# Kernel tuning notes

Hardware: AMD Instinct MI355X
Metric: run time of the kernel (lower is better)

The kernel has to match this reference:

```python
import jax, jax.numpy as jnp
import numpy as np

N = 100000
NEG_SLOPE = 0.2
EPS = 1e-16


def gat_conv(x, edge_index, W, att_src, att_dst, bias, concat):
    # x: [N, Fin]; W: [Fin, H*C]; att_*: [H, C]; edge_index: [2, E] (with self loops)
    H, C = att_src.shape
    src, dst = edge_index[0], edge_index[1]
    h = (x @ W).reshape(-1, H, C)                       # [N, H, C]
    a_src = (h * att_src).sum(-1)                       # [N, H]
    a_dst = (h * att_dst).sum(-1)                       # [N, H]
    e = a_src[src] + a_dst[dst]                         # [E, H]
    e = jnp.where(e >= 0, e, NEG_SLOPE * e)             # LeakyReLU(0.2)
    # segment softmax over destination-node neighborhoods
    m = jax.ops.segment_max(e, dst, num_segments=N)     # [N, H]
    ex = jnp.exp(e - m[dst])
    denom = jax.ops.segment_sum(ex, dst, num_segments=N)
    alpha = ex / (denom[dst] + EPS)                     # [E, H]
    msg = h[src] * alpha[:, :, None]                    # [E, H, C]
    out = jax.ops.segment_sum(msg, dst, num_segments=N)  # [N, H, C]
    out = out.reshape(N, H * C) if concat else out.mean(axis=1)
    return out + bias


def setup_inputs() -> dict:
    key = jax.random.key(0)
    ks = jax.random.split(key, 10)
    Fin, Ch, Co, Hh = 256, 32, 64, 4
    E = 1600000
    x = jax.random.normal(ks[0], (N, Fin), dtype=jnp.float32)
    edge_index = jax.random.randint(ks[1], (2, E), 0, N, dtype=jnp.int64)
    s1 = 1.0 / np.sqrt(Fin)
    s2 = 1.0 / np.sqrt(Hh * Ch)
    W1 = jax.random.normal(ks[2], (Fin, Hh * Ch), dtype=jnp.float32) * s1
    att_src1 = jax.random.normal(ks[3], (Hh, Ch), dtype=jnp.float32) * (1.0 / np.sqrt(Ch))
    att_dst1 = jax.random.normal(ks[4], (Hh, Ch), dtype=jnp.float32) * (1.0 / np.sqrt(Ch))
    b1 = jnp.zeros((Hh * Ch,), dtype=jnp.float32)
    W2 = jax.random.normal(ks[5], (Hh * Ch, Co), dtype=jnp.float32) * s2
    att_src2 = jax.random.normal(ks[6], (1, Co), dtype=jnp.float32) * (1.0 / np.sqrt(Co))
    att_dst2 = jax.random.normal(ks[7], (1, Co), dtype=jnp.float32) * (1.0 / np.sqrt(Co))
    b2 = jnp.zeros((Co,), dtype=jnp.float32)
    return {"x": x, "edge_index": edge_index,
            "W1": W1, "att_src1": att_src1, "att_dst1": att_dst1, "b1": b1,
            "W2": W2, "att_src2": att_src2, "att_dst2": att_dst2, "b2": b2}


def reference(x, edge_index, W1, att_src1, att_dst1, b1, W2, att_src2, att_dst2, b2):
    # add self-loops (PyG GATConv default add_self_loops=True)
    loops = jnp.arange(N, dtype=edge_index.dtype)
    ei = jnp.concatenate([edge_index, jnp.stack([loops, loops])], axis=1)
    h = gat_conv(x, ei, W1, att_src1, att_dst1, b1, concat=True)
    h = jax.nn.elu(h)
    out = gat_conv(h, ei, W2, att_src2, att_dst2, b2, concat=False)
    return out
```

## Files before the change

kernel.cpp:

```cpp
#include <hip/hip_runtime.h>
#include <math.h>

typedef unsigned short ushort_t;
typedef unsigned int uint_t;
typedef __attribute__((ext_vector_type(8))) short short8;
typedef __attribute__((ext_vector_type(4))) float fx4;
typedef __attribute__((ext_vector_type(16))) float f32x16;
typedef __attribute__((ext_vector_type(4))) uint_t uintx4;
typedef __attribute__((ext_vector_type(2))) uint_t uintx2;

__device__ __forceinline__ float bf16_to_f32(ushort_t u) {
    union { uint_t i; float f; } c;
    c.i = ((uint_t)u) << 16;
    return c.f;
}
__device__ __forceinline__ ushort_t f32_to_bf16(float f) {
    union { float f; uint_t i; } c;
    c.f = f;
    const uint_t x = c.i;
    return (ushort_t)((x + 0x7fffu + ((x >> 16) & 1u)) >> 16);
}
__device__ __forceinline__ void unpack_fma(uint_t w, float p, float& a0,
                                           float& a1) {
    union { uint_t i; float f; } lo, hi;
    lo.i = w << 16;
    hi.i = w & 0xffff0000u;
    a0 += p * lo.f;
    a1 += p * hi.f;
}

template <int TILES32, bool A_F32, int K, int KS>
__global__ __launch_bounds__(256) void gemm32_kernel(
    const void* __restrict__ Avoid, const ushort_t* __restrict__ BT,
    ushort_t* __restrict__ C, int n) {
    constexpr int M = TILES32 * 32;
    constexpr int CHS = KS / 8;
    constexpr int NSTEP = KS / 16;
    constexpr int NTOT = K / 16;
    __shared__ ushort_t lds[M * KS];
    const int tid = threadIdx.x;
    const int wave = tid >> 6;
    const int lane = tid & 63;
    const int l31 = lane & 31;
    const int half = lane >> 5;
    const int rowbase = blockIdx.x * 256 + wave * 64;
    const int r0 = min(rowbase + l31, n - 1);
    const int r1 = min(rowbase + 32 + l31, n - 1);
    const size_t off0 = (size_t)r0 * K + half * 8;
    const size_t off1 = (size_t)r1 * K + half * 8;

    f32x16 acc[2][TILES32];
#pragma unroll
    for (int rp = 0; rp < 2; ++rp)
#pragma unroll
        for (int t = 0; t < TILES32; ++t)
#pragma unroll
            for (int i = 0; i < 16; ++i) acc[rp][t][i] = 0.f;

    fx4 c0a, c0b, c1a, c1b, n0a, n0b, n1a, n1b;
    short8 cb0, cb1, nb0, nb1;

    if constexpr (A_F32) {
        const float* A = (const float*)Avoid;
        c0a = *(const fx4*)(A + off0);
        c0b = *(const fx4*)(A + off0 + 4);
        c1a = *(const fx4*)(A + off1);
        c1b = *(const fx4*)(A + off1 + 4);
    } else {
        const ushort_t* A = (const ushort_t*)Avoid;
        cb0 = *(const short8*)(A + off0);
        cb1 = *(const short8*)(A + off1);
    }

#pragma unroll
    for (int ks = 0; ks < K; ks += KS) {
        if (ks) __syncthreads();
#pragma unroll
        for (int i = 0; i < (M * CHS + 255) / 256; ++i) {
            const int idx = tid + i * 256;
            if (idx < M * CHS) {
                const int row = idx / CHS;
                const int c = idx - row * CHS;
                *(short8*)&lds[(size_t)(row * CHS +
                                        (c ^ (row & (CHS - 1)))) * 8] =
                    *(const short8*)(BT + (size_t)row * K + ks + c * 8);
            }
        }
        __syncthreads();

#pragma unroll
        for (int kstep = 0; kstep < NSTEP; ++kstep) {
            const int kg = ks / 16 + kstep;
            if (kg + 1 < NTOT) {
                const int kd = (kg + 1) * 16;
                if constexpr (A_F32) {
                    const float* A = (const float*)Avoid;
                    n0a = *(const fx4*)(A + off0 + kd);
                    n0b = *(const fx4*)(A + off0 + kd + 4);
                    n1a = *(const fx4*)(A + off1 + kd);
                    n1b = *(const fx4*)(A + off1 + kd + 4);
                } else {
                    const ushort_t* A = (const ushort_t*)Avoid;
                    nb0 = *(const short8*)(A + off0 + kd);
                    nb1 = *(const short8*)(A + off1 + kd);
                }
            }
            short8 bf[TILES32];
#pragma unroll
            for (int t = 0; t < TILES32; ++t) {
                const int brow = t * 32 + l31;
                const int c = kstep * 2 + half;
                bf[t] = *(const short8*)&lds[(size_t)(brow * CHS +
                                                      (c ^ (brow &
                                                            (CHS - 1)))) * 8];
            }
            short8 af0, af1;
            if constexpr (A_F32) {
                union { short8 v; ushort_t u[8]; } u0, u1;
#pragma unroll
                for (int j = 0; j < 4; ++j) {
                    u0.u[j] = f32_to_bf16(c0a[j]);
                    u0.u[4 + j] = f32_to_bf16(c0b[j]);
                    u1.u[j] = f32_to_bf16(c1a[j]);
                    u1.u[4 + j] = f32_to_bf16(c1b[j]);
                }
                af0 = u0.v;
                af1 = u1.v;
            } else {
                af0 = cb0;
                af1 = cb1;
            }
#pragma unroll
            for (int t = 0; t < TILES32; ++t) {
                acc[0][t] = __builtin_amdgcn_mfma_f32_32x32x16_bf16(
                    af0, bf[t], acc[0][t], 0, 0, 0);
                acc[1][t] = __builtin_amdgcn_mfma_f32_32x32x16_bf16(
                    af1, bf[t], acc[1][t], 0, 0, 0);
            }
            if (kg + 1 < NTOT) {
                if constexpr (A_F32) {
                    c0a = n0a; c0b = n0b; c1a = n1a; c1b = n1b;
                } else {
                    cb0 = nb0; cb1 = nb1;
                }
            }
        }
    }

#pragma unroll
    for (int rp = 0; rp < 2; ++rp) {
        const int base_r = rowbase + rp * 32 + 4 * half;
#pragma unroll
        for (int t = 0; t < TILES32; ++t) {
            const int col = t * 32 + l31;
#pragma unroll
            for (int reg = 0; reg < 16; ++reg) {
                const int rr = base_r + (reg & 3) + 8 * (reg >> 2);
                if (rr < n)
                    C[(size_t)rr * M + col] = f32_to_bf16(acc[rp][t][reg]);
            }
        }
    }
}

template <int H, int C>
__global__ void att_kernel(const ushort_t* __restrict__ h,
                           const float* __restrict__ att_s,
                           const float* __restrict__ att_d,
                           float* __restrict__ as_, float* __restrict__ ad_,
                           int n) {
    const int idx = blockIdx.x * blockDim.x + threadIdx.x;
    if (idx >= n * H) return;
    const int node = idx / H;
    const int hh = idx % H;
    const ushort_t* hp = h + (size_t)node * H * C + hh * C;
    float s0 = 0.f, s1 = 0.f;
#pragma unroll
    for (int c = 0; c < C; ++c) {
        const float v = bf16_to_f32(hp[c]);
        s0 += v * att_s[hh * C + c];
        s1 += v * att_d[hh * C + c];
    }
    as_[idx] = s0;
    ad_[idx] = s1;
}

__global__ __launch_bounds__(1024) void hist_kernel(
    const int* __restrict__ dst, int* __restrict__ histG, int e, int chunk,
    int NB, int G, const float* __restrict__ W1, ushort_t* __restrict__ W1T,
    const float* __restrict__ W2, ushort_t* __restrict__ W2T) {
    if (blockIdx.x >= (uint_t)G) {
        const int idx = (blockIdx.x - G) * 1024 + threadIdx.x;
        if (idx < 256 * 128) {
            const int mm = idx / 256;
            const int kk = idx - mm * 256;
            W1T[idx] = f32_to_bf16(W1[(size_t)kk * 128 + mm]);
        } else if (idx < 256 * 128 + 128 * 64) {
            const int j = idx - 256 * 128;
            const int mm = j / 128;
            const int kk = j - mm * 128;
            W2T[j] = f32_to_bf16(W2[(size_t)kk * 64 + mm]);
        }
        return;
    }
    __shared__ int hl[512];
    for (int b = threadIdx.x; b < NB; b += 1024) hl[b] = 0;
    __syncthreads();
    const int g = blockIdx.x;
    const int lo = g * chunk;
    const int hi = min(lo + chunk, e);
    for (int i = lo + threadIdx.x; i < hi; i += 1024)
        atomicAdd(&hl[dst[i] >> 8], 1);
    __syncthreads();
    for (int b = threadIdx.x; b < NB; b += 1024) histG[b * G + g] = hl[b];
}

__global__ __launch_bounds__(1024) void scan1_kernel(const int* __restrict__ in,
                                                     int* __restrict__ out,
                                                     int* __restrict__ sums,
                                                     int n) {
    __shared__ int s[1024];
    const int t = threadIdx.x;
    const int i = blockIdx.x * 1024 + t;
    const int v = (i < n) ? in[i] : 0;
    s[t] = v;
    __syncthreads();
    for (int d = 1; d < 1024; d <<= 1) {
        const int x = (t >= d) ? s[t - d] : 0;
        __syncthreads();
        s[t] += x;
        __syncthreads();
    }
    if (i < n) out[i] = s[t] - v;
    if (t == 1023) sums[blockIdx.x] = s[1023];
}

__global__ __launch_bounds__(128) void scan2_kernel(int* sums, int nb) {
    __shared__ int s[128];
    const int t = threadIdx.x;
    const int v = (t < nb) ? sums[t] : 0;
    s[t] = v;
    __syncthreads();
    for (int d = 1; d < 128; d <<= 1) {
        const int x = (t >= d) ? s[t - d] : 0;
        __syncthreads();
        s[t] += x;
        __syncthreads();
    }
    if (t < nb) sums[t] = s[t] - v;
}

__global__ __launch_bounds__(1024) void scan3_kernel(int* __restrict__ out,
                                                     const int* __restrict__ sums,
                                                     int n) {
    const int i = blockIdx.x * 1024 + threadIdx.x;
    if (i < n) out[i] += sums[blockIdx.x];
}

__global__ __launch_bounds__(1024) void bin_kernel(const int* __restrict__ src,
                                                   const int* __restrict__ dst,
                                                   const int* __restrict__ base,
                                                   uint_t* __restrict__ binned,
                                                   int e, int chunk, int NB,
                                                   int G) {
    __shared__ int cur[512];
    const int g = blockIdx.x;
    for (int b = threadIdx.x; b < NB; b += 1024) cur[b] = base[b * G + g];
    __syncthreads();
    const int lo = g * chunk;
    const int hi = min(lo + chunk, e);
    for (int i = lo + threadIdx.x; i < hi; i += 1024) {
        const int d = dst[i];
        const int p = atomicAdd(&cur[d >> 8], 1);
        binned[p] = (uint_t)src[i] | ((uint_t)(d & 255) << 17);
    }
}

#define BUILD_CAP 6144
__global__ __launch_bounds__(256) void build_kernel(
    const uint_t* __restrict__ binned, const int* __restrict__ base,
    int* __restrict__ csr, int* __restrict__ deg, int* __restrict__ offs,
    int e, int n, int NB, int G) {
    __shared__ uint_t ep[BUILD_CAP];
    __shared__ int degL[256];
    __shared__ int offL[256];
    __shared__ int curL[256];
    const int b = blockIdx.x;
    const int tid = threadIdx.x;
    const int start = base[b * G];
    const int end = (b == NB - 1) ? e : base[(b + 1) * G];
    const int cnt = end - start;
    const bool stage = (cnt <= BUILD_CAP);
    degL[tid] = 0;
    if (stage)
        for (int i = tid; i < cnt; i += 256) ep[i] = binned[start + i];
    __syncthreads();
    if (stage) {
        for (int i = tid; i < cnt; i += 256)
            atomicAdd(&degL[ep[i] >> 17], 1);
    } else {
        for (int i = tid; i < cnt; i += 256)
            atomicAdd(&degL[binned[start + i] >> 17], 1);
    }
    __syncthreads();
    const int v = degL[tid];
    offL[tid] = v;
    __syncthreads();
    for (int d = 1; d < 256; d <<= 1) {
        const int x = (tid >= d) ? offL[tid - d] : 0;
        __syncthreads();
        offL[tid] += x;
        __syncthreads();
    }
    const int excl = offL[tid] - v;
    curL[tid] = excl;
    const int node = (b << 8) + tid;
    if (node < n) {
        deg[node] = v;
        offs[node] = start + excl;
    }
    __syncthreads();
    if (stage) {
        for (int i = tid; i < cnt; i += 256) {
            const uint_t pr = ep[i];
            const int p = atomicAdd(&curL[pr >> 17], 1);
            csr[start + p] = (int)(pr & 0x1FFFFu);
        }
    } else {
        for (int i = tid; i < cnt; i += 256) {
            const uint_t pr = binned[start + i];
            const int p = atomicAdd(&curL[pr >> 17], 1);
            csr[start + p] = (int)(pr & 0x1FFFFu);
        }
    }
}

template <int H, int C, bool DO_ELU, bool OUT_BF16>
__global__ __launch_bounds__(64) void agg_kernel(
    const ushort_t* __restrict__ h, const float* __restrict__ a_src,
    const float* __restrict__ a_dst, const int* __restrict__ csr,
    const int* __restrict__ offs, const int* __restrict__ deg,
    const float* __restrict__ bias, void* __restrict__ outv, int n0, int n1,
    int n) {
    constexpr int HC = H * C;
    constexpr int R = HC / 16;
    constexpr int RW = R / 2;
    constexpr int U = 4;
    const int lane = threadIdx.x;
    const int s = lane & 15;
    const int g = lane >> 4;
    const int dst = n0 + blockIdx.x * 4 + g;
    const int dstc = min(dst, n - 1);
    const int start = offs[dstc];
    const int dg = deg[dstc];
    const int ch0 = s * R;
    const int myh = (H > 1) ? (ch0 / C) : 0;
    const float advm = a_dst[dstc * H + myh];

    int dmax = dg;
    dmax = max(dmax, __shfl_xor(dmax, 16));
    dmax = max(dmax, __shfl_xor(dmax, 32));
    dmax = __builtin_amdgcn_readfirstlane(dmax);

    float acc[R];
#pragma unroll
    for (int r = 0; r < R; ++r) acc[r] = 0.f;
    float L = 0.f;

    {
        float e = a_src[dstc * H + myh] + advm;
        e = fmaxf(e, 0.2f * e);
        const float p = __expf(e);
        L += p;
        const ushort_t* hp = h + (size_t)((uint_t)dstc * HC) + ch0;
        if constexpr (RW == 4) {
            const uintx4 v = *(const uintx4*)hp;
#pragma unroll
            for (int w = 0; w < 4; ++w)
                unpack_fma(v[w], p, acc[2 * w], acc[2 * w + 1]);
        } else {
            const uintx2 v = *(const uintx2*)hp;
#pragma unroll
            for (int w = 0; w < 2; ++w)
                unpack_fma(v[w], p, acc[2 * w], acc[2 * w + 1]);
        }
    }

    const int dm1c = (dg > 0) ? dg - 1 : 0;

    for (int j0 = 0; j0 < dmax; j0 += U) {
        int sv[U];
#pragma unroll
        for (int u = 0; u < U; ++u)
            sv[u] = csr[start + min(j0 + u, dm1c)];
        float es[U];
#pragma unroll
        for (int u = 0; u < U; ++u) es[u] = a_src[sv[u] * H + myh];
        uint_t hv[U][RW];
#pragma unroll
        for (int u = 0; u < U; ++u) {
            const ushort_t* hp = h + (size_t)((uint_t)sv[u] * HC) + ch0;
            if constexpr (RW == 4) {
                const uintx4 v = *(const uintx4*)hp;
#pragma unroll
                for (int w = 0; w < 4; ++w) hv[u][w] = v[w];
            } else {
                const uintx2 v = *(const uintx2*)hp;
#pragma unroll
                for (int w = 0; w < 2; ++w) hv[u][w] = v[w];
            }
        }
        float p[U];
#pragma unroll
        for (int u = 0; u < U; ++u) {
            float e = es[u] + advm;
            e = fmaxf(e, 0.2f * e);
            const float pe = __expf(e);
            p[u] = (j0 + u < dg) ? pe : 0.f;
        }
#pragma unroll
        for (int u = 0; u < U; ++u) {
            L += p[u];
#pragma unroll
            for (int w = 0; w < RW; ++w)
                unpack_fma(hv[u][w], p[u], acc[2 * w], acc[2 * w + 1]);
        }
    }

    if (dst >= n1) return;
    const float linv = 1.f / (L + 1e-16f);
    float r[R];
#pragma unroll
    for (int d = 0; d < R; ++d) {
        r[d] = acc[d] * linv + bias[ch0 + d];
        if (DO_ELU) r[d] = (r[d] > 0.f) ? r[d] : (__expf(r[d]) - 1.f);
    }
    if constexpr (OUT_BF16) {
        uintx4 o;
#pragma unroll
        for (int w = 0; w < 4; ++w)
            o[w] = (uint_t)f32_to_bf16(r[2 * w]) |
                   ((uint_t)f32_to_bf16(r[2 * w + 1]) << 16);
        *(uintx4*)((ushort_t*)outv + (size_t)dst * HC + ch0) = o;
    } else {
        fx4 o;
#pragma unroll
        for (int d = 0; d < 4; ++d) o[d] = r[d];
        *(fx4*)((float*)outv + (size_t)dst * HC + ch0) = o;
    }
}

extern "C" void kernel_launch(void* const* d_in, const int* in_sizes, int n_in,
                              void* d_out, int out_size, void* d_ws,
                              size_t ws_size, hipStream_t stream) {
    const float* x = (const float*)d_in[0];
    const int* ei = (const int*)d_in[1];
    const float* W1 = (const float*)d_in[2];
    const float* att_s1 = (const float*)d_in[3];
    const float* att_d1 = (const float*)d_in[4];
    const float* b1 = (const float*)d_in[5];
    const float* W2 = (const float*)d_in[6];
    const float* att_s2 = (const float*)d_in[7];
    const float* att_d2 = (const float*)d_in[8];
    const float* b2 = (const float*)d_in[9];

    const int N = in_sizes[0] / 256;
    const int E = in_sizes[1] / 2;
    const int* srcp = ei;
    const int* dstp = ei + E;

    const int NB = (N + 255) >> 8;
    const int G = 128;
    const int NBG = NB * G;
    const int chunk = (E + G - 1) / G;
    const int nbs = (NBG + 1023) / 1024;

    float* as1 = (float*)d_ws;
    float* ad1 = as1 + (size_t)N * 4;
    float* as2 = ad1 + (size_t)N * 4;
    float* ad2 = as2 + N;
    int* histG = (int*)(ad2 + N);
    int* base = histG + NBG;
    int* sums = base + NBG;
    int* deg = sums + 128;
    int* offs = deg + N;
    int* csr = offs + N;
    uint_t* binned = (uint_t*)(csr + E);
    ushort_t* h1 = (ushort_t*)binned;
    ushort_t* h2 = h1 + (size_t)N * 128;
    ushort_t* h1p = h2 + (size_t)N * 64;
    ushort_t* W1T = h1p + (size_t)N * 128;
    ushort_t* W2T = W1T + 128 * 256;

    const int cvblk = (256 * 128 + 128 * 64 + 1023) / 1024;
    hist_kernel<<<G + cvblk, 1024, 0, stream>>>(dstp, histG, E, chunk, NB, G,
                                                W1, W1T, W2, W2T);
    scan1_kernel<<<nbs, 1024, 0, stream>>>(histG, base, sums, NBG);
    scan2_kernel<<<1, 128, 0, stream>>>(sums, nbs);
    scan3_kernel<<<nbs, 1024, 0, stream>>>(base, sums, NBG);
    bin_kernel<<<G, 1024, 0, stream>>>(srcp, dstp, base, binned, E, chunk, NB,
                                       G);
    build_kernel<<<NB, 256, 0, stream>>>(binned, base, csr, deg, offs, E, N,
                                         NB, G);

    const int gblk = (N + 255) / 256;

    gemm32_kernel<4, true, 256, 128><<<gblk, 256, 0, stream>>>(x, W1T, h1, N);
    att_kernel<4, 32><<<(N * 4 + 255) / 256, 256, 0, stream>>>(h1, att_s1,
                                                               att_d1, as1,
                                                               ad1, N);
    {
        const int part = (N + 2) / 3;
        for (int p = 0; p < 3; ++p) {
            const int lo = p * part;
            const int hi = min(lo + part, N);
            if (hi > lo)
                agg_kernel<4, 32, true, true>
                    <<<(hi - lo + 3) / 4, 64, 0, stream>>>(
                        h1, as1, ad1, csr, offs, deg, b1, h1p, lo, hi, N);
        }
    }

    gemm32_kernel<2, false, 128, 128><<<gblk, 256, 0, stream>>>(h1p, W2T, h2,
                                                                N);
    att_kernel<1, 64><<<(N + 255) / 256, 256, 0, stream>>>(h2, att_s2, att_d2,
                                                           as2, ad2, N);
    agg_kernel<1, 64, false, false><<<(N + 3) / 4, 64, 0, stream>>>(
        h2, as2, ad2, csr, offs, deg, b2, d_out, 0, N, N);
}
```

Before: 394.8 us.

## Fuse attention-score dot products into GEMM epilogue and merge scan/agg launches

Computes the per-node source and destination attention scores inside the GEMM epilogue, using shuffle reductions over the fp32 accumulators. This removes the separate att_kernel passes that re-read h from memory. It also folds the scan2 step into scan3 with a per-block wave reduction, and launches the layer-1 aggregation as one kernel instead of three partitions. The cost is extra shuffles and register pressure in the GEMM epilogue. The scores now come from fp32 accumulators rather than bf16-rounded h, which changes them slightly.

```diff
diff --git a/kernel.cpp b/kernel.cpp
--- a/kernel.cpp
+++ b/kernel.cpp
@@ -29,10 +29,12 @@
     a1 += p * hi.f;
 }
 
-template <int TILES32, bool A_F32, int K, int KS>
+template <int TILES32, bool A_F32, int K, int KS, int HATT>
 __global__ __launch_bounds__(256) void gemm32_kernel(
     const void* __restrict__ Avoid, const ushort_t* __restrict__ BT,
-    ushort_t* __restrict__ C, int n) {
+    ushort_t* __restrict__ C, const float* __restrict__ att_s,
+    const float* __restrict__ att_d, float* __restrict__ as_,
+    float* __restrict__ ad_, int n) {
     constexpr int M = TILES32 * 32;
     constexpr int CHS = KS / 8;
     constexpr int NSTEP = KS / 16;
@@ -147,42 +149,59 @@
         }
     }
 
+    float satt_s[TILES32], satt_d[TILES32];
+#pragma unroll
+    for (int t = 0; t < TILES32; ++t) {
+        satt_s[t] = att_s[t * 32 + l31];
+        satt_d[t] = att_d[t * 32 + l31];
+    }
 #pragma unroll
     for (int rp = 0; rp < 2; ++rp) {
         const int base_r = rowbase + rp * 32 + 4 * half;
 #pragma unroll
-        for (int t = 0; t < TILES32; ++t) {
-            const int col = t * 32 + l31;
-#pragma unroll
-            for (int reg = 0; reg < 16; ++reg) {
-                const int rr = base_r + (reg & 3) + 8 * (reg >> 2);
-                if (rr < n)
-                    C[(size_t)rr * M + col] = f32_to_bf16(acc[rp][t][reg]);
-            }
-        }
-    }
-}
-
-template <int H, int C>
-__global__ void att_kernel(const ushort_t* __restrict__ h,
-                           const float* __restrict__ att_s,
-                           const float* __restrict__ att_d,
-                           float* __restrict__ as_, float* __restrict__ ad_,
-                           int n) {
-    const int idx = blockIdx.x * blockDim.x + threadIdx.x;
-    if (idx >= n * H) return;
-    const int node = idx / H;
-    const int hh = idx % H;
-    const ushort_t* hp = h + (size_t)node * H * C + hh * C;
-    float s0 = 0.f, s1 = 0.f;
-#pragma unroll
-    for (int c = 0; c < C; ++c) {
-        const float v = bf16_to_f32(hp[c]);
-        s0 += v * att_s[hh * C + c];
-        s1 += v * att_d[hh * C + c];
-    }
-    as_[idx] = s0;
-    ad_[idx] = s1;
+        for (int reg = 0; reg < 16; ++reg) {
+            const int rr = base_r + (reg & 3) + 8 * (reg >> 2);
+            float vs[TILES32], vd[TILES32];
+#pragma unroll
+            for (int t = 0; t < TILES32; ++t) {
+                vs[t] = acc[rp][t][reg] * satt_s[t];
+                vd[t] = acc[rp][t][reg] * satt_d[t];
+            }
+            constexpr int NH = (HATT == 1) ? 1 : TILES32;
+            if constexpr (HATT == 1) {
+#pragma unroll
+                for (int t = 1; t < TILES32; ++t) {
+                    vs[0] += vs[t];
+                    vd[0] += vd[t];
+                }
+            }
+#pragma unroll
+            for (int d = 1; d < 32; d <<= 1) {
+#pragma unroll
+                for (int hh = 0; hh < NH; ++hh) {
+                    vs[hh] += __shfl_xor(vs[hh], d);
+                    vd[hh] += __shfl_xor(vd[hh], d);
+                }
+            }
+            if (l31 == 0 && rr < n) {
+                if constexpr (HATT == 4) {
+                    *(fx4*)(as_ + (size_t)rr * 4) =
+                        (fx4){vs[0], vs[1], vs[2], vs[3]};
+                    *(fx4*)(ad_ + (size_t)rr * 4) =
+                        (fx4){vd[0], vd[1], vd[2], vd[3]};
+                } else {
+                    as_[rr] = vs[0];
+                    ad_[rr] = vd[0];
+                }
+            }
+            if (rr < n) {
+#pragma unroll
+                for (int t = 0; t < TILES32; ++t)
+                    C[(size_t)rr * M + t * 32 + l31] =
+                        f32_to_bf16(acc[rp][t][reg]);
+            }
+        }
+    }
 }
 
 __global__ __launch_bounds__(1024) void hist_kernel(
@@ -235,26 +254,19 @@
     if (t == 1023) sums[blockIdx.x] = s[1023];
 }
 
-__global__ __launch_bounds__(128) void scan2_kernel(int* sums, int nb) {
-    __shared__ int s[128];
-    const int t = threadIdx.x;
-    const int v = (t < nb) ? sums[t] : 0;
-    s[t] = v;
-    __syncthreads();
-    for (int d = 1; d < 128; d <<= 1) {
-        const int x = (t >= d) ? s[t - d] : 0;
-        __syncthreads();
-        s[t] += x;
-        __syncthreads();
-    }
-    if (t < nb) sums[t] = s[t] - v;
-}
-
-__global__ __launch_bounds__(1024) void scan3_kernel(int* __restrict__ out,
-                                                     const int* __restrict__ sums,
-                                                     int n) {
+__global__ __launch_bounds__(1024) void scan3_kernel(
+    int* __restrict__ out, const int* __restrict__ sums, int n, int nb) {
+    __shared__ int offsh;
+    if (threadIdx.x < 64) {
+        const int t = threadIdx.x;
+        int v = (t < nb && t < (int)blockIdx.x) ? sums[t] : 0;
+#pragma unroll
+        for (int d = 1; d < 64; d <<= 1) v += __shfl_xor(v, d);
+        if (t == 0) offsh = v;
+    }
+    __syncthreads();
     const int i = blockIdx.x * 1024 + threadIdx.x;
-    if (i < n) out[i] += sums[blockIdx.x];
+    if (i < n) out[i] += offsh;
 }
 
 __global__ __launch_bounds__(1024) void bin_kernel(const int* __restrict__ src,
@@ -340,8 +352,7 @@
     const ushort_t* __restrict__ h, const float* __restrict__ a_src,
     const float* __restrict__ a_dst, const int* __restrict__ csr,
     const int* __restrict__ offs, const int* __restrict__ deg,
-    const float* __restrict__ bias, void* __restrict__ outv, int n0, int n1,
-    int n) {
+    const float* __restrict__ bias, void* __restrict__ outv, int n) {
     constexpr int HC = H * C;
     constexpr int R = HC / 16;
     constexpr int RW = R / 2;
@@ -349,7 +360,7 @@
     const int lane = threadIdx.x;
     const int s = lane & 15;
     const int g = lane >> 4;
-    const int dst = n0 + blockIdx.x * 4 + g;
+    const int dst = blockIdx.x * 4 + g;
     const int dstc = min(dst, n - 1);
     const int start = offs[dstc];
     const int dg = deg[dstc];
@@ -427,7 +438,7 @@
         }
     }
 
-    if (dst >= n1) return;
+    if (dst >= n) return;
     const float linv = 1.f / (L + 1e-16f);
     float r[R];
 #pragma unroll
@@ -496,35 +507,23 @@
     hist_kernel<<<G + cvblk, 1024, 0, stream>>>(dstp, histG, E, chunk, NB, G,
                                                 W1, W1T, W2, W2T);
     scan1_kernel<<<nbs, 1024, 0, stream>>>(histG, base, sums, NBG);
-    scan2_kernel<<<1, 128, 0, stream>>>(sums, nbs);
-    scan3_kernel<<<nbs, 1024, 0, stream>>>(base, sums, NBG);
+    scan3_kernel<<<nbs, 1024, 0, stream>>>(base, sums, NBG, nbs);
     bin_kernel<<<G, 1024, 0, stream>>>(srcp, dstp, base, binned, E, chunk, NB,
                                        G);
     build_kernel<<<NB, 256, 0, stream>>>(binned, base, csr, deg, offs, E, N,
                                          NB, G);
 
     const int gblk = (N + 255) / 256;
-
-    gemm32_kernel<4, true, 256, 128><<<gblk, 256, 0, stream>>>(x, W1T, h1, N);
-    att_kernel<4, 32><<<(N * 4 + 255) / 256, 256, 0, stream>>>(h1, att_s1,
-                                                               att_d1, as1,
-                                                               ad1, N);
-    {
-        const int part = (N + 2) / 3;
-        for (int p = 0; p < 3; ++p) {
-            const int lo = p * part;
-            const int hi = min(lo + part, N);
-            if (hi > lo)
-                agg_kernel<4, 32, true, true>
-                    <<<(hi - lo + 3) / 4, 64, 0, stream>>>(
-                        h1, as1, ad1, csr, offs, deg, b1, h1p, lo, hi, N);
-        }
-    }
-
-    gemm32_kernel<2, false, 128, 128><<<gblk, 256, 0, stream>>>(h1p, W2T, h2,
-                                                                N);
-    att_kernel<1, 64><<<(N + 255) / 256, 256, 0, stream>>>(h2, att_s2, att_d2,
-                                                           as2, ad2, N);
-    agg_kernel<1, 64, false, false><<<(N + 3) / 4, 64, 0, stream>>>(
-        h2, as2, ad2, csr, offs, deg, b2, d_out, 0, N, N);
-}
+    const int ablk = (N + 3) / 4;
+
+    gemm32_kernel<4, true, 256, 128, 4><<<gblk, 256, 0, stream>>>(
+        x, W1T, h1, att_s1, att_d1, as1, ad1, N);
+    agg_kernel<4, 32, true, true><<<ablk, 64, 0, stream>>>(h1, as1, ad1, csr,
+                                                           offs, deg, b1, h1p,
+                                                           N);
+
+    gemm32_kernel<2, false, 128, 128, 1><<<gblk, 256, 0, stream>>>(
+        h1p, W2T, h2, att_s2, att_d2, as2, ad2, N);
+    agg_kernel<1, 64, false, false><<<ablk, 64, 0, stream>>>(
+        h2, as2, ad2, csr, offs, deg, b2, d_out, N);
+}
```

Result: no change. 396.9 us (+0.5%).
